# Performance work log

Measured on AMD Instinct MI355X. Metric: run time of the kernel, lower is better.

## Reference

```python
import jax, jax.numpy as jnp
import numpy as np
import math

D, H, DK, F, V, L = 512, 8, 64, 2048, 8192, 2
B, S, T = 16, 128, 128
EPS = 1e-5


def _ln(x, g, b):
    mu = jnp.mean(x, -1, keepdims=True)
    var = jnp.mean((x - mu) ** 2, -1, keepdims=True)
    return g * (x - mu) * jax.lax.rsqrt(var + EPS) + b


def _pe(length):
    pos = jnp.arange(length, dtype=jnp.float32)[:, None]
    div = jnp.exp(jnp.arange(0, D, 2, dtype=jnp.float32) * (-math.log(10000.0) / D))
    ang = pos * div
    pe = jnp.zeros((length, D), jnp.float32)
    return pe.at[:, 0::2].set(jnp.sin(ang)).at[:, 1::2].set(jnp.cos(ang))


def _attn(q, k, v, src, dst, num_dst):
    # per-edge score = exp(clip((k_src . q_dst)/sqrt(d_k), -5, 5))  [E, H]
    score = jnp.einsum('ehd,ehd->eh', k[src], q[dst]) / math.sqrt(DK)
    score = jnp.exp(jnp.clip(score, -5.0, 5.0))
    wv = jax.ops.segment_sum(v[src] * score[..., None], dst, num_segments=num_dst)
    z = jax.ops.segment_sum(score, dst, num_segments=num_dst)
    return (wv / z[..., None]).reshape(num_dst, D)


def _forward(src_tokens, tgt_tokens, ee_src, ee_dst, dd_src, dd_dst, ed_src, ed_dst, P):
    (src_emb, tgt_emb, eW, eB, elg, elb, eW1, eb1, eW2, eb2, eng, enb,
     dsW, dsB, dcW, dcB, dlg, dlb, dW1, db1, dW2, db2, dng, dnb, gW, gb) = P
    pe = _pe(max(S, T))
    Ne, Nd = B * S, B * T
    xe = (src_emb[src_tokens] * math.sqrt(D) + pe[None, :S]).reshape(Ne, D)
    xd = (tgt_emb[tgt_tokens] * math.sqrt(D) + pe[None, :T]).reshape(Nd, D)
    # encoder stack
    for i in range(L):
        nx = _ln(xe, elg[i, 0], elb[i, 0])
        q = (nx @ eW[i, 0] + eB[i, 0]).reshape(Ne, H, DK)
        k = (nx @ eW[i, 1] + eB[i, 1]).reshape(Ne, H, DK)
        v = (nx @ eW[i, 2] + eB[i, 2]).reshape(Ne, H, DK)
        xe = xe + _attn(q, k, v, ee_src, ee_dst, Ne) @ eW[i, 3] + eB[i, 3]
        nx = _ln(xe, elg[i, 1], elb[i, 1])
        xe = xe + jax.nn.relu(nx @ eW1[i] + eb1[i]) @ eW2[i] + eb2[i]
        if i == L - 1:
            xe = _ln(xe, eng, enb)
    # decoder stack
    for i in range(L):
        nx = _ln(xd, dlg[i, 0], dlb[i, 0])
        q = (nx @ dsW[i, 0] + dsB[i, 0]).reshape(Nd, H, DK)
        k = (nx @ dsW[i, 1] + dsB[i, 1]).reshape(Nd, H, DK)
        v = (nx @ dsW[i, 2] + dsB[i, 2]).reshape(Nd, H, DK)
        xd = xd + _attn(q, k, v, dd_src, dd_dst, Nd) @ dsW[i, 3] + dsB[i, 3]
        nq = _ln(xd, dlg[i, 1], dlb[i, 1])
        nkv = _ln(xe, dlg[i, 1], dlb[i, 1])
        q = (nq @ dcW[i, 0] + dcB[i, 0]).reshape(Nd, H, DK)
        k = (nkv @ dcW[i, 1] + dcB[i, 1]).reshape(Ne, H, DK)
        v = (nkv @ dcW[i, 2] + dcB[i, 2]).reshape(Ne, H, DK)
        xd = xd + _attn(q, k, v, ed_src, ed_dst, Nd) @ dcW[i, 3] + dcB[i, 3]
        nx = _ln(xd, dlg[i, 2], dlb[i, 2])
        xd = xd + jax.nn.relu(nx @ dW1[i] + db1[i]) @ dW2[i] + db2[i]
        if i == L - 1:
            xd = _ln(xd, dng, dnb)
    return jax.nn.log_softmax(xd @ gW + gb, axis=-1)  # [Nd, V]


def setup_inputs() -> dict:
    key = jax.random.key(0)
    ks = iter(jax.random.split(key, 40))
    def nrm(shape, scale=0.02):
        return jax.random.normal(next(ks), shape, dtype=jnp.float32) * scale
    src_tokens = jax.random.randint(next(ks), (B, S), 0, V, dtype=jnp.int32)
    tgt_tokens = jax.random.randint(next(ks), (B, T), 0, V, dtype=jnp.int32)
    # graph structure (per-sentence blocks)
    si, di = np.meshgrid(np.arange(S), np.arange(S), indexing='ij')
    si, di = si.ravel(), di.ravel()
    base = (np.arange(B) * S)[:, None]
    ee_src = (base + si[None, :]).ravel().astype(np.int32)
    ee_dst = (base + di[None, :]).ravel().astype(np.int32)
    m = si <= di  # causal: src pos <= dst pos
    dd_src = (base + si[m][None, :]).ravel().astype(np.int32)
    dd_dst = (base + di[m][None, :]).ravel().astype(np.int32)
    ed_src = ee_src.copy()
    ed_dst = ee_dst.copy()
    inp = dict(
        src_tokens=src_tokens, tgt_tokens=tgt_tokens,
        ee_src=jnp.asarray(ee_src), ee_dst=jnp.asarray(ee_dst),
        dd_src=jnp.asarray(dd_src), dd_dst=jnp.asarray(dd_dst),
        ed_src=jnp.asarray(ed_src), ed_dst=jnp.asarray(ed_dst),
        src_emb=nrm((V, D), 1.0 / math.sqrt(D)), tgt_emb=nrm((V, D), 1.0 / math.sqrt(D)),
        enc_attn_W=nrm((L, 4, D, D)), enc_attn_b=jnp.zeros((L, 4, D), jnp.float32),
        enc_ln_g=jnp.ones((L, 2, D), jnp.float32), enc_ln_b=jnp.zeros((L, 2, D), jnp.float32),
        enc_ff_W1=nrm((L, D, F)), enc_ff_b1=jnp.zeros((L, F), jnp.float32),
        enc_ff_W2=nrm((L, F, D)), enc_ff_b2=jnp.zeros((L, D), jnp.float32),
        enc_norm_g=jnp.ones((D,), jnp.float32), enc_norm_b=jnp.zeros((D,), jnp.float32),
        dec_self_W=nrm((L, 4, D, D)), dec_self_b=jnp.zeros((L, 4, D), jnp.float32),
        dec_cross_W=nrm((L, 4, D, D)), dec_cross_b=jnp.zeros((L, 4, D), jnp.float32),
        dec_ln_g=jnp.ones((L, 3, D), jnp.float32), dec_ln_b=jnp.zeros((L, 3, D), jnp.float32),
        dec_ff_W1=nrm((L, D, F)), dec_ff_b1=jnp.zeros((L, F), jnp.float32),
        dec_ff_W2=nrm((L, F, D)), dec_ff_b2=jnp.zeros((L, D), jnp.float32),
        dec_norm_g=jnp.ones((D,), jnp.float32), dec_norm_b=jnp.zeros((D,), jnp.float32),
        gen_W=nrm((D, V)), gen_b=jnp.zeros((V,), jnp.float32),
    )
    return inp


def reference(src_tokens, tgt_tokens, ee_src, ee_dst, dd_src, dd_dst, ed_src, ed_dst,
              src_emb, tgt_emb, enc_attn_W, enc_attn_b, enc_ln_g, enc_ln_b,
              enc_ff_W1, enc_ff_b1, enc_ff_W2, enc_ff_b2, enc_norm_g, enc_norm_b,
              dec_self_W, dec_self_b, dec_cross_W, dec_cross_b, dec_ln_g, dec_ln_b,
              dec_ff_W1, dec_ff_b1, dec_ff_W2, dec_ff_b2, dec_norm_g, dec_norm_b,
              gen_W, gen_b):
    P = (src_emb, tgt_emb, enc_attn_W, enc_attn_b, enc_ln_g, enc_ln_b,
         enc_ff_W1, enc_ff_b1, enc_ff_W2, enc_ff_b2, enc_norm_g, enc_norm_b,
         dec_self_W, dec_self_b, dec_cross_W, dec_cross_b, dec_ln_g, dec_ln_b,
         dec_ff_W1, dec_ff_b1, dec_ff_W2, dec_ff_b2, dec_norm_g, dec_norm_b, gen_W, gen_b)
    return _forward(src_tokens, tgt_tokens, ee_src, ee_dst, dd_src, dd_dst, ed_src, ed_dst, P)
```

## Files before the change

kernel.cpp:

```cpp
#include <hip/hip_runtime.h>

typedef __attribute__((ext_vector_type(8))) short bfx8;
typedef __attribute__((ext_vector_type(4))) float fx4;

static __device__ __forceinline__ unsigned short f2bf(float f) {
    union { float f; unsigned int u; } v; v.f = f;
    unsigned int i = v.u;
    return (unsigned short)((i + 0x7FFFu + ((i >> 16) & 1u)) >> 16);
}
static __device__ __forceinline__ float bf2f(unsigned short u) {
    union { unsigned int ui; float f; } cv;
    cv.ui = ((unsigned int)u) << 16;
    return cv.f;
}

static __device__ __forceinline__ void gl2lds16(const unsigned short* g, unsigned short* l) {
    unsigned long long gu = (unsigned long long)g;
    unsigned int lu = (unsigned int)(unsigned long long)l;
    __builtin_amdgcn_global_load_lds(
        (const __attribute__((address_space(1))) void*)gu,
        (__attribute__((address_space(3))) void*)lu,
        16, 0, 0);
}

struct TrGroup {
    const float* src;
    unsigned short* dst;
    int srcRowStride;
    int dstRowStride;
    long srcSliceOff;
    long dstSliceOff;
};
struct TrTable {
    TrGroup g[18];
    int zStart[19];
};

__global__ __launch_bounds__(256) void trall_kernel(TrTable tt)
{
    __shared__ unsigned short tile[32][33];
    int z = blockIdx.z;
    int gi = 0;
#pragma unroll 1
    while (z >= tt.zStart[gi + 1]) ++gi;
    int zi = z - tt.zStart[gi];
    const float* s = tt.g[gi].src + (size_t)zi * tt.g[gi].srcSliceOff;
    unsigned short* d = tt.g[gi].dst + (size_t)zi * tt.g[gi].dstSliceOff;
    int srs = tt.g[gi].srcRowStride, drs = tt.g[gi].dstRowStride;
    int n0 = blockIdx.x * 32, k0 = blockIdx.y * 32;
    int tx = threadIdx.x & 31, ty = threadIdx.x >> 5;
#pragma unroll
    for (int i = 0; i < 32; i += 8)
        tile[ty + i][tx] = f2bf(s[(size_t)(k0 + ty + i) * srs + (n0 + tx)]);
    __syncthreads();
#pragma unroll
    for (int i = 0; i < 32; i += 8)
        d[(size_t)(n0 + ty + i) * drs + (k0 + tx)] = tile[tx][ty + i];
}

__global__ __launch_bounds__(256) void embed2_kernel(
    const int* __restrict__ tokA, const int* __restrict__ tokB,
    const float* __restrict__ embA, const float* __restrict__ embB,
    float* __restrict__ outA, float* __restrict__ outB)
{
    int idx = blockIdx.x;
    int row = idx & 2047;
    const int* tok = idx < 2048 ? tokA : tokB;
    const float* emb = idx < 2048 ? embA : embB;
    float* out = idx < 2048 ? outA : outB;
    int pos = row & 127;
    int t = tok[row];
    for (int d = threadIdx.x; d < 512; d += 256) {
        float ang = (float)pos * expf((float)(d & ~1) * (-9.210340371976184f / 512.0f));
        float pe = (d & 1) ? cosf(ang) : sinf(ang);
        out[(size_t)row * 512 + d] = emb[(size_t)t * 512 + d] * 22.627416997969522f + pe;
    }
}

static __device__ __forceinline__ void ln_row(
    const float* __restrict__ xrow, const float* __restrict__ g,
    const float* __restrict__ b, int lane, fx4& o0, fx4& o1)
{
    const fx4* xr = (const fx4*)xrow;
    fx4 a = xr[lane * 2], c = xr[lane * 2 + 1];
    float s = a[0] + a[1] + a[2] + a[3] + c[0] + c[1] + c[2] + c[3];
#pragma unroll
    for (int off = 32; off; off >>= 1) s += __shfl_xor(s, off);
    float mu = s * (1.0f / 512.0f);
    float qv = 0.f;
#pragma unroll
    for (int j = 0; j < 4; ++j) {
        float d0 = a[j] - mu; qv += d0 * d0;
        float d1 = c[j] - mu; qv += d1 * d1;
    }
#pragma unroll
    for (int off = 32; off; off >>= 1) qv += __shfl_xor(qv, off);
    float rs = rsqrtf(qv * (1.0f / 512.0f) + 1e-5f);
    const fx4* gr = (const fx4*)g;
    const fx4* br = (const fx4*)b;
    fx4 g0 = gr[lane * 2], g1 = gr[lane * 2 + 1];
    fx4 b0 = br[lane * 2], b1 = br[lane * 2 + 1];
#pragma unroll
    for (int j = 0; j < 4; ++j) {
        o0[j] = g0[j] * (a[j] - mu) * rs + b0[j];
        o1[j] = g1[j] * (c[j] - mu) * rs + b1[j];
    }
}

template<bool OUTBF>
__global__ __launch_bounds__(256) void ln_kernel(
    const float* __restrict__ x, const float* __restrict__ g,
    const float* __restrict__ b, void* __restrict__ out)
{
    int row = blockIdx.x * 4 + (threadIdx.x >> 6);
    int lane = threadIdx.x & 63;
    fx4 o0, o1;
    ln_row(x + (size_t)row * 512, g, b, lane, o0, o1);
    if (OUTBF) {
        unsigned short* orow = (unsigned short*)out + (size_t)row * 512 + lane * 8;
        ushort4 u0 = {f2bf(o0[0]), f2bf(o0[1]), f2bf(o0[2]), f2bf(o0[3])};
        ushort4 u1 = {f2bf(o1[0]), f2bf(o1[1]), f2bf(o1[2]), f2bf(o1[3])};
        *(ushort4*)orow = u0;
        *(ushort4*)(orow + 4) = u1;
    } else {
        fx4* orow = (fx4*)out + (size_t)row * 128;
        orow[lane * 2] = o0;
        orow[lane * 2 + 1] = o1;
    }
}

__global__ __launch_bounds__(256) void ln2_kernel(
    const float* __restrict__ x0, const float* __restrict__ x1,
    const float* __restrict__ g, const float* __restrict__ b,
    unsigned short* __restrict__ o0, unsigned short* __restrict__ o1)
{
    int idx = blockIdx.x * 4 + (threadIdx.x >> 6);
    int lane = threadIdx.x & 63;
    const float* x = idx < 2048 ? x0 : x1;
    unsigned short* o = idx < 2048 ? o0 : o1;
    int row = idx & 2047;
    fx4 v0, v1;
    ln_row(x + (size_t)row * 512, g, b, lane, v0, v1);
    unsigned short* orow = o + (size_t)row * 512 + lane * 8;
    ushort4 u0 = {f2bf(v0[0]), f2bf(v0[1]), f2bf(v0[2]), f2bf(v0[3])};
    ushort4 u1 = {f2bf(v1[0]), f2bf(v1[1]), f2bf(v1[2]), f2bf(v1[3])};
    *(ushort4*)orow = u0;
    *(ushort4*)(orow + 4) = u1;
}

template<bool RELU, bool RESID, bool OUTBF>
__global__ __launch_bounds__(256) void gemm_bk128_kernel(
    const unsigned short* __restrict__ A, const unsigned short* __restrict__ Wt,
    const float* __restrict__ bias, const float* __restrict__ res,
    void* __restrict__ Cv, int K, int ldc, int gx)
{
    __shared__ unsigned short smem[2][2][8192];
    const int tid = threadIdx.x;
    const int nwg = gridDim.x;
    const int cpx = nwg >> 3;
    const int phys = blockIdx.x;
    const int logical = (phys & 7) * cpx + (phys >> 3);
    const int bm = (logical / gx) * 64;
    const int bn = (logical % gx) * 64;
    const int lane = tid & 63;
    const int wv = tid >> 6;
    const int wr = (wv >> 1) * 32;
    const int wc = (wv & 1) * 32;
    const int lr = lane & 15;
    const int lrow4 = lane >> 4;
    const int lchk16 = lane & 15;
    fx4 acc00 = {0.f, 0.f, 0.f, 0.f}, acc01 = {0.f, 0.f, 0.f, 0.f};
    fx4 acc10 = {0.f, 0.f, 0.f, 0.f}, acc11 = {0.f, 0.f, 0.f, 0.f};

    auto stage = [&](int buf, int k0) {
#pragma unroll
        for (int j = 0; j < 4; ++j) {
            int row = wv * 16 + j * 4 + lrow4;
            int sc = (lchk16 ^ (row & 15)) * 8;
            gl2lds16(A + (size_t)(bm + row) * K + k0 + sc,
                     &smem[buf][0][(wv * 16 + j * 4) * 128]);
            gl2lds16(Wt + (size_t)(bn + row) * K + k0 + sc,
                     &smem[buf][1][(wv * 16 + j * 4) * 128]);
        }
    };

    const int nt = K >> 7;
    int cur = 0;
    stage(0, 0);
    for (int t = 0; t < nt; ++t) {
        __syncthreads();
        if (t + 1 < nt) stage(cur ^ 1, (t + 1) << 7);
        const unsigned short* bufA = &smem[cur][0][0];
        const unsigned short* bufB = &smem[cur][1][0];
        const int ra0 = wr + lr, ra1 = wr + 16 + lr;
        const int rb0 = wc + lr, rb1 = wc + 16 + lr;
        __builtin_amdgcn_s_setprio(1);
#pragma unroll
        for (int kk = 0; kk < 4; ++kk) {
            int ca = kk * 4 + (lane >> 4);
            bfx8 a0 = *(const bfx8*)&bufA[ra0 * 128 + ((ca ^ (ra0 & 15)) * 8)];
            bfx8 a1 = *(const bfx8*)&bufA[ra1 * 128 + ((ca ^ (ra1 & 15)) * 8)];
            bfx8 b0 = *(const bfx8*)&bufB[rb0 * 128 + ((ca ^ (rb0 & 15)) * 8)];
            bfx8 b1 = *(const bfx8*)&bufB[rb1 * 128 + ((ca ^ (rb1 & 15)) * 8)];
            acc00 = __builtin_amdgcn_mfma_f32_16x16x32_bf16(a0, b0, acc00, 0, 0, 0);
            acc01 = __builtin_amdgcn_mfma_f32_16x16x32_bf16(a0, b1, acc01, 0, 0, 0);
            acc10 = __builtin_amdgcn_mfma_f32_16x16x32_bf16(a1, b0, acc10, 0, 0, 0);
            acc11 = __builtin_amdgcn_mfma_f32_16x16x32_bf16(a1, b1, acc11, 0, 0, 0);
        }
        __builtin_amdgcn_s_setprio(0);
        cur ^= 1;
    }
    int rbase = bm + wr + ((lane >> 4) * 4);
    int cbase = bn + wc + lr;
#pragma unroll
    for (int m = 0; m < 2; ++m) {
        fx4 am0 = m ? acc10 : acc00;
        fx4 am1 = m ? acc11 : acc01;
#pragma unroll
        for (int r = 0; r < 4; ++r) {
            int row = rbase + m * 16 + r;
#pragma unroll
            for (int half = 0; half < 2; ++half) {
                int col = cbase + half * 16;
                float v = (half ? am1[r] : am0[r]) + bias[col];
                if (RESID) v += res[(size_t)row * ldc + col];
                if (RELU) v = fmaxf(v, 0.f);
                if (OUTBF) ((unsigned short*)Cv)[(size_t)row * ldc + col] = f2bf(v);
                else       ((float*)Cv)[(size_t)row * ldc + col] = v;
            }
        }
    }
}

template<bool RELU>
__global__ __launch_bounds__(256) void gemm128_kernel(
    const unsigned short* __restrict__ A, const unsigned short* __restrict__ Wt,
    const float* __restrict__ bias, unsigned short* __restrict__ C,
    int K, int ldc)
{
    __shared__ unsigned short smem[2][2][8192];
    const int tid = threadIdx.x;
    const int nwg = gridDim.x;
    const int cpx = nwg >> 3;
    const int phys = blockIdx.x;
    const int logical = (phys & 7) * cpx + (phys >> 3);
    const int bm = (logical & 15) * 128;
    const int bn = (logical >> 4) * 128;
    const int lane = tid & 63;
    const int wv = tid >> 6;
    const int wr = (wv >> 1) * 64;
    const int wc = (wv & 1) * 64;
    const int lr = lane & 15;
    const int lrow = lane >> 3;
    const int lchk = lane & 7;
    fx4 acc[4][4];
#pragma unroll
    for (int mi = 0; mi < 4; ++mi)
#pragma unroll
        for (int ni = 0; ni < 4; ++ni) acc[mi][ni] = fx4{0.f, 0.f, 0.f, 0.f};

    auto stage = [&](int buf, int k0) {
#pragma unroll
        for (int j = 0; j < 4; ++j) {
            int row = wv * 32 + j * 8 + lrow;
            int sc = lchk ^ (row & 7);
            gl2lds16(A + (size_t)(bm + row) * K + k0 + sc * 8,
                     &smem[buf][0][(wv * 32 + j * 8) * 64]);
            gl2lds16(Wt + (size_t)(bn + row) * K + k0 + sc * 8,
                     &smem[buf][1][(wv * 32 + j * 8) * 64]);
        }
    };

    const int nt = K >> 6;
    int cur = 0;
    stage(0, 0);
    for (int t = 0; t < nt; ++t) {
        __syncthreads();
        if (t + 1 < nt) stage(cur ^ 1, (t + 1) << 6);
        const unsigned short* bufA = &smem[cur][0][0];
        const unsigned short* bufB = &smem[cur][1][0];
        __builtin_amdgcn_s_setprio(1);
#pragma unroll
        for (int kk = 0; kk < 2; ++kk) {
            int ca = kk * 4 + (lane >> 4);
            bfx8 af[4], bg[4];
#pragma unroll
            for (int i = 0; i < 4; ++i) {
                int ra = wr + i * 16 + lr;
                int rb = wc + i * 16 + lr;
                af[i] = *(const bfx8*)&bufA[ra * 64 + ((ca ^ (ra & 7)) * 8)];
                bg[i] = *(const bfx8*)&bufB[rb * 64 + ((ca ^ (rb & 7)) * 8)];
            }
#pragma unroll
            for (int mi = 0; mi < 4; ++mi)
#pragma unroll
                for (int ni = 0; ni < 4; ++ni)
                    acc[mi][ni] = __builtin_amdgcn_mfma_f32_16x16x32_bf16(af[mi], bg[ni], acc[mi][ni], 0, 0, 0);
        }
        __builtin_amdgcn_s_setprio(0);
        cur ^= 1;
    }
    int rbase = bm + wr + ((lane >> 4) * 4);
    int cbase = bn + wc + lr;
#pragma unroll
    for (int mi = 0; mi < 4; ++mi)
#pragma unroll
        for (int ni = 0; ni < 4; ++ni) {
            int col = cbase + ni * 16;
            float bv = bias[col];
#pragma unroll
            for (int r = 0; r < 4; ++r) {
                int row = rbase + mi * 16 + r;
                float v = acc[mi][ni][r] + bv;
                if (RELU) v = fmaxf(v, 0.f);
                C[(size_t)row * ldc + col] = f2bf(v);
            }
        }
}

template<bool CAUSAL, bool SELF>
__global__ __launch_bounds__(512) void fattn_kernel(
    const unsigned short* __restrict__ xq, const unsigned short* __restrict__ xkv,
    const unsigned short* __restrict__ Wt, const float* __restrict__ bias,
    unsigned short* __restrict__ out)
{
    constexpr int XROWS = SELF ? 128 : 192;
    constexpr int BUFB  = (XROWS + 192) * 64 * 2;
    __shared__ __align__(16) unsigned char lds[2 * BUFB + 9216 + 18432 + 17408 + 512];
    const int blk = blockIdx.x;
    const int half = blk & 1;
    const int h = (blk >> 1) & 7;
    const int b = blk >> 4;
    const int q0 = half * 64;
    const int tid = threadIdx.x;
    const int lane = tid & 63;
    const int wv = tid >> 6;
    const int lr = lane & 15;
    const int hg8 = (lane >> 4) * 8;
    const int rloc = (lane >> 4) * 4;
    const int lrow = lane >> 3;
    const int lchk = lane & 7;

    const unsigned short* gxq = xq + (size_t)(b * 128 + q0) * 512;
    const unsigned short* gkv = xkv + (size_t)(b * 128) * 512;
    const unsigned short* gw  = Wt + (size_t)(h * 64) * 512;

    auto stage = [&](int buf, int k0) {
        unsigned short* dst = (unsigned short*)(lds + buf * BUFB);
        if constexpr (SELF) {
#pragma unroll
            for (int j = 0; j < 5; ++j) {
                int start = wv * 40 + j * 8;
                int row = start + lrow;
                int sc = (lchk ^ (row & 7)) * 8;
                const unsigned short* src;
                if (start < 128) {
                    src = gkv + (size_t)row * 512 + k0 + sc;
                } else {
                    int wr_ = row - 128;
                    src = gw + ((size_t)(wr_ & 63) + (size_t)(wr_ >> 6) * 512) * 512 + k0 + sc;
                }
                gl2lds16(src, dst + start * 64);
            }
        } else {
            unsigned short* dstW = dst + XROWS * 64;
#pragma unroll
            for (int j = 0; j < 3; ++j) {
                int row = wv * 24 + j * 8 + lrow;
                int sc = (lchk ^ (row & 7)) * 8;
                const unsigned short* xs = (row < 64)
                    ? gxq + (size_t)row * 512
                    : gkv + (size_t)(row - 64) * 512;
                gl2lds16(xs + k0 + sc, dst + (wv * 24 + j * 8) * 64);
                const unsigned short* ws = gw + ((size_t)(row & 63) + (size_t)(row >> 6) * 512) * 512;
                gl2lds16(ws + k0 + sc, dstW + (wv * 24 + j * 8) * 64);
            }
        }
    };

    fx4 accQ[4], accK[4], accV[4];
#pragma unroll
    for (int c = 0; c < 4; ++c) {
        accQ[c] = fx4{0.f, 0.f, 0.f, 0.f};
        accK[c] = fx4{0.f, 0.f, 0.f, 0.f};
        accV[c] = fx4{0.f, 0.f, 0.f, 0.f};
    }
    stage(0, 0);
#pragma unroll 1
    for (int t = 0; t < 8; ++t) {
        __syncthreads();
        if (t < 7) stage((t + 1) & 1, (t + 1) * 64);
        const unsigned short* stX = (const unsigned short*)(lds + (t & 1) * BUFB);
        const unsigned short* stW = stX + XROWS * 64;
#pragma unroll
        for (int kk = 0; kk < 2; ++kk) {
            const int ca = kk * 4 + (lane >> 4);
            auto rd = [&](const unsigned short* base, int row) -> bfx8 {
                return *(const bfx8*)(base + row * 64 + ((ca ^ (row & 7)) * 8));
            };
            const int kvbase = SELF ? 0 : 64;
            bfx8 aKV = rd(stX, kvbase + wv * 16 + lr);
            bfx8 aQ = aKV;
            if (wv >= 4) aQ = rd(stX, (SELF ? q0 : 0) + (wv - 4) * 16 + lr);
            __builtin_amdgcn_s_setprio(1);
#pragma unroll
            for (int c = 0; c < 4; ++c) {
                bfx8 bk = rd(stW, 64 + c * 16 + lr);
                accK[c] = __builtin_amdgcn_mfma_f32_16x16x32_bf16(aKV, bk, accK[c], 0, 0, 0);
                bfx8 bv = rd(stW, 128 + c * 16 + lr);
                accV[c] = __builtin_amdgcn_mfma_f32_16x16x32_bf16(aKV, bv, accV[c], 0, 0, 0);
                if (wv >= 4) {
                    bfx8 bq = rd(stW, c * 16 + lr);
                    accQ[c] = __builtin_amdgcn_mfma_f32_16x16x32_bf16(aQ, bq, accQ[c], 0, 0, 0);
                }
            }
            __builtin_amdgcn_s_setprio(0);
        }
    }
    unsigned short* sQ  = (unsigned short*)(lds + 2 * BUFB);
    unsigned short* sK  = (unsigned short*)(lds + 2 * BUFB + 9216);
    unsigned short* sVt = (unsigned short*)(lds + 2 * BUFB + 9216 + 18432);
    float* zp = (float*)(lds + 2 * BUFB + 9216 + 18432 + 17408);
    unsigned short* sP  = (unsigned short*)lds;
#pragma unroll
    for (int c = 0; c < 4; ++c) {
        int col = c * 16 + lr;
        float bk_ = bias[512 + h * 64 + col];
        float bv_ = bias[1024 + h * 64 + col];
#pragma unroll
        for (int r = 0; r < 4; ++r) {
            sK[(wv * 16 + rloc + r) * 72 + col] = f2bf(accK[c][r] + bk_);
            sVt[col * 136 + (wv * 16 + rloc + r)] = f2bf(accV[c][r] + bv_);
        }
        if (wv >= 4) {
            float bq_ = bias[h * 64 + col];
#pragma unroll
            for (int r = 0; r < 4; ++r)
                sQ[((wv - 4) * 16 + rloc + r) * 72 + col] = f2bf(accQ[c][r] + bq_);
        }
    }
    __syncthreads();
    const int qb = wv >> 1;
    const int kh = wv & 1;
    fx4 acc[4];
#pragma unroll
    for (int n = 0; n < 4; ++n) acc[n] = fx4{0.f, 0.f, 0.f, 0.f};
#pragma unroll
    for (int kk = 0; kk < 2; ++kk) {
        bfx8 a = *(const bfx8*)(sQ + (qb * 16 + lr) * 72 + kk * 32 + hg8);
#pragma unroll
        for (int n = 0; n < 4; ++n) {
            bfx8 bb = *(const bfx8*)(sK + ((kh * 4 + n) * 16 + lr) * 72 + kk * 32 + hg8);
            acc[n] = __builtin_amdgcn_mfma_f32_16x16x32_bf16(a, bb, acc[n], 0, 0, 0);
        }
    }
    const int qg = q0 + qb * 16 + rloc;
#pragma unroll
    for (int r = 0; r < 4; ++r) {
        float zs = 0.f;
#pragma unroll
        for (int n = 0; n < 4; ++n) {
            float s = acc[n][r] * 0.125f;
            s = __expf(fminf(fmaxf(s, -5.f), 5.f));
            if (CAUSAL && (kh * 64 + n * 16 + lr) > (qg + r)) s = 0.f;
            zs += s;
            sP[(qb * 16 + rloc + r) * 136 + kh * 64 + n * 16 + lr] = f2bf(s);
        }
#pragma unroll
        for (int off = 8; off; off >>= 1) zs += __shfl_xor(zs, off);
        if (lr == 0) zp[(qb * 2 + kh) * 16 + rloc + r] = zs;
    }
    __syncthreads();
    float zinv[4];
#pragma unroll
    for (int r = 0; r < 4; ++r)
        zinv[r] = 1.f / (zp[(qb * 2 + 0) * 16 + rloc + r] + zp[(qb * 2 + 1) * 16 + rloc + r]);
    const int dh = wv & 1;
    fx4 acc2[2];
    acc2[0] = fx4{0.f, 0.f, 0.f, 0.f};
    acc2[1] = fx4{0.f, 0.f, 0.f, 0.f};
#pragma unroll
    for (int kk = 0; kk < 4; ++kk) {
        bfx8 a = *(const bfx8*)(sP + (qb * 16 + lr) * 136 + kk * 32 + hg8);
#pragma unroll
        for (int dn = 0; dn < 2; ++dn) {
            bfx8 bb = *(const bfx8*)(sVt + (dh * 32 + dn * 16 + lr) * 136 + kk * 32 + hg8);
            acc2[dn] = __builtin_amdgcn_mfma_f32_16x16x32_bf16(a, bb, acc2[dn], 0, 0, 0);
        }
    }
#pragma unroll
    for (int dn = 0; dn < 2; ++dn)
#pragma unroll
        for (int r = 0; r < 4; ++r) {
            size_t row = (size_t)(b * 128 + qg + r);
            out[row * 512 + h * 64 + dh * 32 + dn * 16 + lr] = f2bf(acc2[dn][r] * zinv[r]);
        }
}

__global__ __launch_bounds__(256) void logsoftmax_bf16_kernel(
    const unsigned short* __restrict__ logits, float* __restrict__ out)
{
    __shared__ float red[4];
    int tid = threadIdx.x;
    const bfx8* lrow = (const bfx8*)(logits + (size_t)blockIdx.x * 8192);
    float* orow = out + (size_t)blockIdx.x * 8192;
    float vals[32];
    float mx = -1e30f;
#pragma unroll
    for (int i = 0; i < 4; ++i) {
        bfx8 u = lrow[i * 256 + tid];
#pragma unroll
        for (int j = 0; j < 8; ++j) {
            float f = bf2f((unsigned short)u[j]);
            vals[i * 8 + j] = f;
            mx = fmaxf(mx, f);
        }
    }
#pragma unroll
    for (int off = 32; off; off >>= 1) mx = fmaxf(mx, __shfl_xor(mx, off));
    int wid = tid >> 6;
    if ((tid & 63) == 0) red[wid] = mx;
    __syncthreads();
    mx = fmaxf(fmaxf(red[0], red[1]), fmaxf(red[2], red[3]));
    __syncthreads();
    float sum = 0.f;
#pragma unroll
    for (int i = 0; i < 32; ++i) sum += __expf(vals[i] - mx);
#pragma unroll
    for (int off = 32; off; off >>= 1) sum += __shfl_xor(sum, off);
    if ((tid & 63) == 0) red[wid] = sum;
    __syncthreads();
    sum = red[0] + red[1] + red[2] + red[3];
    float lsub = mx + logf(sum);
#pragma unroll
    for (int i = 0; i < 4; ++i) {
        fx4 o0, o1;
#pragma unroll
        for (int j = 0; j < 4; ++j) {
            o0[j] = vals[i * 8 + j] - lsub;
            o1[j] = vals[i * 8 + 4 + j] - lsub;
        }
        ((fx4*)orow)[(i * 256 + tid) * 2] = o0;
        ((fx4*)orow)[(i * 256 + tid) * 2 + 1] = o1;
    }
}

extern "C" void kernel_launch(void* const* d_in, const int* in_sizes, int n_in,
                              void* d_out, int out_size, void* d_ws, size_t ws_size,
                              hipStream_t stream) {
    (void)in_sizes; (void)n_in; (void)out_size; (void)ws_size;
    const int* src_tokens = (const int*)d_in[0];
    const int* tgt_tokens = (const int*)d_in[1];
    const float* src_emb    = (const float*)d_in[8];
    const float* tgt_emb    = (const float*)d_in[9];
    const float* enc_attn_W = (const float*)d_in[10];
    const float* enc_attn_b = (const float*)d_in[11];
    const float* enc_ln_g   = (const float*)d_in[12];
    const float* enc_ln_b   = (const float*)d_in[13];
    const float* enc_ff_W1  = (const float*)d_in[14];
    const float* enc_ff_b1  = (const float*)d_in[15];
    const float* enc_ff_W2  = (const float*)d_in[16];
    const float* enc_ff_b2  = (const float*)d_in[17];
    const float* enc_norm_g = (const float*)d_in[18];
    const float* enc_norm_b = (const float*)d_in[19];
    const float* dec_self_W = (const float*)d_in[20];
    const float* dec_self_b = (const float*)d_in[21];
    const float* dec_cross_W= (const float*)d_in[22];
    const float* dec_cross_b= (const float*)d_in[23];
    const float* dec_ln_g   = (const float*)d_in[24];
    const float* dec_ln_b   = (const float*)d_in[25];
    const float* dec_ff_W1  = (const float*)d_in[26];
    const float* dec_ff_b1  = (const float*)d_in[27];
    const float* dec_ff_W2  = (const float*)d_in[28];
    const float* dec_ff_b2  = (const float*)d_in[29];
    const float* dec_norm_g = (const float*)d_in[30];
    const float* dec_norm_b = (const float*)d_in[31];
    const float* gen_W      = (const float*)d_in[32];
    const float* gen_b      = (const float*)d_in[33];
    float* dout = (float*)d_out;

    unsigned short* wt = (unsigned short*)d_ws;
    const size_t OFF_ENCQKV = 0;
    const size_t OFF_ENCO   = 1572864;
    const size_t OFF_ENCW1  = 2097152;
    const size_t OFF_ENCW2  = 4194304;
    const size_t OFF_DECSQKV= 6291456;
    const size_t OFF_DECSO  = 7864320;
    const size_t OFF_DECCQKV= 8388608;
    const size_t OFF_DECCO  = 9961472;
    const size_t OFF_DECW1  = 10485760;
    const size_t OFF_DECW2  = 12582912;
    const size_t OFF_GENW   = 14680064;
    const size_t WT_ELEMS   = 18874368;
    float* fb  = (float*)(wt + WT_ELEMS);
    float* xe  = fb;
    float* xd  = fb + 1048576;
    unsigned short* nxb  = (unsigned short*)(fb + 2097152);
    unsigned short* nkvb = (unsigned short*)(fb + 3145728);
    unsigned short* ffb  = (unsigned short*)(fb + 4194304);
    unsigned short* attb = (unsigned short*)(fb + 7340032);
    unsigned short* genin   = (unsigned short*)fb;
    unsigned short* logitsb = (unsigned short*)(fb + 1048576);

    TrTable tt;
    {
        int z = 0, gi = 0;
        auto addg = [&](const float* s, unsigned short* d, int srs, int drs,
                        long so, long dof, int zc) {
            tt.zStart[gi] = z;
            tt.g[gi].src = s; tt.g[gi].dst = d;
            tt.g[gi].srcRowStride = srs; tt.g[gi].dstRowStride = drs;
            tt.g[gi].srcSliceOff = so; tt.g[gi].dstSliceOff = dof;
            ++gi; z += zc;
        };
        addg(enc_attn_W,              wt + OFF_ENCQKV,               512,  512,  262144,    262144, 3);
        addg(enc_attn_W + 4L*262144,  wt + OFF_ENCQKV + 3L*262144,   512,  512,  262144,    262144, 3);
        addg(enc_attn_W + 3L*262144,  wt + OFF_ENCO,                 512,  512,  4L*262144, 262144, 2);
        addg(enc_ff_W1,               wt + OFF_ENCW1,                2048, 512,  512,       262144, 4);
        addg(enc_ff_W1 + 1048576,     wt + OFF_ENCW1 + 1048576,      2048, 512,  512,       262144, 4);
        addg(enc_ff_W2,               wt + OFF_ENCW2,                512,  2048, 262144,    512,    4);
        addg(enc_ff_W2 + 1048576,     wt + OFF_ENCW2 + 1048576,      512,  2048, 262144,    512,    4);
        addg(dec_self_W,              wt + OFF_DECSQKV,              512,  512,  262144,    262144, 3);
        addg(dec_self_W + 4L*262144,  wt + OFF_DECSQKV + 3L*262144,  512,  512,  262144,    262144, 3);
        addg(dec_self_W + 3L*262144,  wt + OFF_DECSO,                512,  512,  4L*262144, 262144, 2);
        addg(dec_cross_W,             wt + OFF_DECCQKV,              512,  512,  262144,    262144, 3);
        addg(dec_cross_W + 4L*262144, wt + OFF_DECCQKV + 3L*262144,  512,  512,  262144,    262144, 3);
        addg(dec_cross_W + 3L*262144, wt + OFF_DECCO,                512,  512,  4L*262144, 262144, 2);
        addg(dec_ff_W1,               wt + OFF_DECW1,                2048, 512,  512,       262144, 4);
        addg(dec_ff_W1 + 1048576,     wt + OFF_DECW1 + 1048576,      2048, 512,  512,       262144, 4);
        addg(dec_ff_W2,               wt + OFF_DECW2,                512,  2048, 262144,    512,    4);
        addg(dec_ff_W2 + 1048576,     wt + OFF_DECW2 + 1048576,      512,  2048, 262144,    512,    4);
        addg(gen_W,                   wt + OFF_GENW,                 8192, 512,  512,       262144, 16);
        tt.zStart[18] = z;
    }
    trall_kernel<<<dim3(16, 16, 72), 256, 0, stream>>>(tt);

    embed2_kernel<<<4096, 256, 0, stream>>>(src_tokens, tgt_tokens, src_emb, tgt_emb, xe, xd);

    auto gemmK = [&](const unsigned short* A, const unsigned short* W, const float* bias,
                     const float* res, void* C, int N, int K, int ldc, bool relu, bool outbf) {
        int gx = N / 64;
        dim3 g(gx * 32);
        if (res)        gemm_bk128_kernel<false, true,  false><<<g, 256, 0, stream>>>(A, W, bias, res, C, K, ldc, gx);
        else if (relu)  gemm_bk128_kernel<true,  false, true ><<<g, 256, 0, stream>>>(A, W, bias, res, C, K, ldc, gx);
        else if (outbf) gemm_bk128_kernel<false, false, true ><<<g, 256, 0, stream>>>(A, W, bias, res, C, K, ldc, gx);
        else            gemm_bk128_kernel<false, false, false><<<g, 256, 0, stream>>>(A, W, bias, res, C, K, ldc, gx);
    };
    auto gemm128 = [&](const unsigned short* A, const unsigned short* W, const float* bias,
                       unsigned short* C, int N, int K, int ldc, bool relu) {
        dim3 g((N / 128) * 16);
        if (relu) gemm128_kernel<true ><<<g, 256, 0, stream>>>(A, W, bias, C, K, ldc);
        else      gemm128_kernel<false><<<g, 256, 0, stream>>>(A, W, bias, C, K, ldc);
    };
    auto lnb = [&](const float* x, const float* g, const float* b, unsigned short* o) {
        ln_kernel<true><<<512, 256, 0, stream>>>(x, g, b, o);
    };
    auto lnf = [&](const float* x, const float* g, const float* b, float* o) {
        ln_kernel<false><<<512, 256, 0, stream>>>(x, g, b, o);
    };

    for (int i = 0; i < 2; ++i) {
        lnb(xe, enc_ln_g + (size_t)(i * 2 + 0) * 512, enc_ln_b + (size_t)(i * 2 + 0) * 512, nxb);
        fattn_kernel<false, true><<<256, 512, 0, stream>>>(
            nxb, nxb, wt + OFF_ENCQKV + (size_t)i * 3 * 262144,
            enc_attn_b + (size_t)i * 4 * 512, attb);
        gemmK(attb, wt + OFF_ENCO + (size_t)i * 262144, enc_attn_b + (size_t)i * 4 * 512 + 1536,
              xe, xe, 512, 512, 512, false, false);
        lnb(xe, enc_ln_g + (size_t)(i * 2 + 1) * 512, enc_ln_b + (size_t)(i * 2 + 1) * 512, nxb);
        gemm128(nxb, wt + OFF_ENCW1 + (size_t)i * 1048576, enc_ff_b1 + (size_t)i * 2048,
                ffb, 2048, 512, 2048, true);
        gemmK(ffb, wt + OFF_ENCW2 + (size_t)i * 1048576, enc_ff_b2 + (size_t)i * 512,
              xe, xe, 512, 2048, 512, false, false);
    }
    lnf(xe, enc_norm_g, enc_norm_b, xe);

    for (int i = 0; i < 2; ++i) {
        lnb(xd, dec_ln_g + (size_t)(i * 3 + 0) * 512, dec_ln_b + (size_t)(i * 3 + 0) * 512, nxb);
        fattn_kernel<true, true><<<256, 512, 0, stream>>>(
            nxb, nxb, wt + OFF_DECSQKV + (size_t)i * 3 * 262144,
            dec_self_b + (size_t)i * 4 * 512, attb);
        gemmK(attb, wt + OFF_DECSO + (size_t)i * 262144, dec_self_b + (size_t)i * 4 * 512 + 1536,
              xd, xd, 512, 512, 512, false, false);
        ln2_kernel<<<1024, 256, 0, stream>>>(
            xd, xe, dec_ln_g + (size_t)(i * 3 + 1) * 512, dec_ln_b + (size_t)(i * 3 + 1) * 512,
            nxb, nkvb);
        fattn_kernel<false, false><<<256, 512, 0, stream>>>(
            nxb, nkvb, wt + OFF_DECCQKV + (size_t)i * 3 * 262144,
            dec_cross_b + (size_t)i * 4 * 512, attb);
        gemmK(attb, wt + OFF_DECCO + (size_t)i * 262144, dec_cross_b + (size_t)i * 4 * 512 + 1536,
              xd, xd, 512, 512, 512, false, false);
        lnb(xd, dec_ln_g + (size_t)(i * 3 + 2) * 512, dec_ln_b + (size_t)(i * 3 + 2) * 512, nxb);
        gemm128(nxb, wt + OFF_DECW1 + (size_t)i * 1048576, dec_ff_b1 + (size_t)i * 2048,
                ffb, 2048, 512, 2048, true);
        gemmK(ffb, wt + OFF_DECW2 + (size_t)i * 1048576, dec_ff_b2 + (size_t)i * 512,
              xd, xd, 512, 2048, 512, false, false);
    }
    lnb(xd, dec_norm_g, dec_norm_b, genin);

    gemm128(genin, wt + OFF_GENW, gen_b, logitsb, 8192, 512, 8192, false);
    logsoftmax_bf16_kernel<<<2048, 256, 0, stream>>>(logitsb, dout);
}
```

Measured before the change: 336.7 us.

## Fuse LayerNorm into embedding, output-projection GEMMs, and encoder final norm

Embedding now also computes the first encoder and decoder LayerNorms. A new full-row GEMM kernel (64x512 tile) fuses bias, residual and the following LayerNorm for the attention output projections. The encoder final norm also produces both decoder cross-attention K/V LayerNorm outputs up front. This removes several separate LN launches and the re-read of the residual stream. In exchange, the fused GEMM launches only 32 workgroups, which may underuse the GPU, and it computes variance as E[x²]−mu² in single-pass form.

```diff
diff --git a/kernel.cpp b/kernel.cpp
--- a/kernel.cpp
+++ b/kernel.cpp
@@ -58,23 +58,51 @@
         d[(size_t)(n0 + ty + i) * drs + (k0 + tx)] = tile[tx][ty + i];
 }
 
-__global__ __launch_bounds__(256) void embed2_kernel(
+__global__ __launch_bounds__(256) void embedln_kernel(
     const int* __restrict__ tokA, const int* __restrict__ tokB,
     const float* __restrict__ embA, const float* __restrict__ embB,
-    float* __restrict__ outA, float* __restrict__ outB)
+    float* __restrict__ outA, float* __restrict__ outB,
+    const float* __restrict__ gA, const float* __restrict__ bA,
+    const float* __restrict__ gB, const float* __restrict__ bB,
+    unsigned short* __restrict__ nxA, unsigned short* __restrict__ nxB)
 {
+    __shared__ float red[4];
     int idx = blockIdx.x;
     int row = idx & 2047;
-    const int* tok = idx < 2048 ? tokA : tokB;
-    const float* emb = idx < 2048 ? embA : embB;
-    float* out = idx < 2048 ? outA : outB;
+    bool e = idx < 2048;
+    const int* tok = e ? tokA : tokB;
+    const float* emb = e ? embA : embB;
+    float* out = e ? outA : outB;
+    const float* g = e ? gA : gB;
+    const float* bb = e ? bA : bB;
+    unsigned short* nx = e ? nxA : nxB;
     int pos = row & 127;
     int t = tok[row];
-    for (int d = threadIdx.x; d < 512; d += 256) {
+    int d0 = threadIdx.x, d1 = threadIdx.x + 256;
+    auto pe = [&](int d) {
         float ang = (float)pos * expf((float)(d & ~1) * (-9.210340371976184f / 512.0f));
-        float pe = (d & 1) ? cosf(ang) : sinf(ang);
-        out[(size_t)row * 512 + d] = emb[(size_t)t * 512 + d] * 22.627416997969522f + pe;
-    }
+        return (d & 1) ? cosf(ang) : sinf(ang);
+    };
+    float v0 = emb[(size_t)t * 512 + d0] * 22.627416997969522f + pe(d0);
+    float v1 = emb[(size_t)t * 512 + d1] * 22.627416997969522f + pe(d1);
+    out[(size_t)row * 512 + d0] = v0;
+    out[(size_t)row * 512 + d1] = v1;
+    int lane = threadIdx.x & 63, wv = threadIdx.x >> 6;
+    float s = v0 + v1;
+#pragma unroll
+    for (int off = 32; off; off >>= 1) s += __shfl_xor(s, off);
+    if (lane == 0) red[wv] = s;
+    __syncthreads();
+    float mu = (red[0] + red[1] + red[2] + red[3]) * (1.0f / 512.0f);
+    __syncthreads();
+    float q = (v0 - mu) * (v0 - mu) + (v1 - mu) * (v1 - mu);
+#pragma unroll
+    for (int off = 32; off; off >>= 1) q += __shfl_xor(q, off);
+    if (lane == 0) red[wv] = q;
+    __syncthreads();
+    float rs = rsqrtf((red[0] + red[1] + red[2] + red[3]) * (1.0f / 512.0f) + 1e-5f);
+    nx[(size_t)row * 512 + d0] = f2bf(g[d0] * (v0 - mu) * rs + bb[d0]);
+    nx[(size_t)row * 512 + d1] = f2bf(g[d1] * (v1 - mu) * rs + bb[d1]);
 }
 
 static __device__ __forceinline__ void ln_row(
@@ -129,23 +157,51 @@
     }
 }
 
-__global__ __launch_bounds__(256) void ln2_kernel(
-    const float* __restrict__ x0, const float* __restrict__ x1,
-    const float* __restrict__ g, const float* __restrict__ b,
-    unsigned short* __restrict__ o0, unsigned short* __restrict__ o1)
+__global__ __launch_bounds__(256) void ln3_kernel(
+    float* __restrict__ xe, const float* __restrict__ eg, const float* __restrict__ eb,
+    const float* __restrict__ g0, const float* __restrict__ b0,
+    const float* __restrict__ g1, const float* __restrict__ b1,
+    unsigned short* __restrict__ nk0, unsigned short* __restrict__ nk1)
 {
-    int idx = blockIdx.x * 4 + (threadIdx.x >> 6);
+    int row = blockIdx.x * 4 + (threadIdx.x >> 6);
     int lane = threadIdx.x & 63;
-    const float* x = idx < 2048 ? x0 : x1;
-    unsigned short* o = idx < 2048 ? o0 : o1;
-    int row = idx & 2047;
-    fx4 v0, v1;
-    ln_row(x + (size_t)row * 512, g, b, lane, v0, v1);
-    unsigned short* orow = o + (size_t)row * 512 + lane * 8;
-    ushort4 u0 = {f2bf(v0[0]), f2bf(v0[1]), f2bf(v0[2]), f2bf(v0[3])};
-    ushort4 u1 = {f2bf(v1[0]), f2bf(v1[1]), f2bf(v1[2]), f2bf(v1[3])};
-    *(ushort4*)orow = u0;
-    *(ushort4*)(orow + 4) = u1;
+    fx4 t0, t1;
+    ln_row(xe + (size_t)row * 512, eg, eb, lane, t0, t1);
+    fx4* orow = (fx4*)(xe + (size_t)row * 512);
+    orow[lane * 2] = t0;
+    orow[lane * 2 + 1] = t1;
+    float s = t0[0] + t0[1] + t0[2] + t0[3] + t1[0] + t1[1] + t1[2] + t1[3];
+#pragma unroll
+    for (int off = 32; off; off >>= 1) s += __shfl_xor(s, off);
+    float mu = s * (1.0f / 512.0f);
+    float q = 0.f;
+#pragma unroll
+    for (int j = 0; j < 4; ++j) {
+        float a = t0[j] - mu; q += a * a;
+        float c = t1[j] - mu; q += c * c;
+    }
+#pragma unroll
+    for (int off = 32; off; off >>= 1) q += __shfl_xor(q, off);
+    float rs = rsqrtf(q * (1.0f / 512.0f) + 1e-5f);
+    const fx4* g0r = (const fx4*)g0; const fx4* b0r = (const fx4*)b0;
+    const fx4* g1r = (const fx4*)g1; const fx4* b1r = (const fx4*)b1;
+    fx4 ga0 = g0r[lane * 2], ga1 = g0r[lane * 2 + 1];
+    fx4 bb0 = b0r[lane * 2], bb1 = b0r[lane * 2 + 1];
+    fx4 gc0 = g1r[lane * 2], gc1 = g1r[lane * 2 + 1];
+    fx4 bc0 = b1r[lane * 2], bc1 = b1r[lane * 2 + 1];
+    unsigned short* o0 = nk0 + (size_t)row * 512 + lane * 8;
+    unsigned short* o1 = nk1 + (size_t)row * 512 + lane * 8;
+    ushort4 ua0, ua1, uc0, uc1;
+#pragma unroll
+    for (int j = 0; j < 4; ++j) {
+        float n0 = (t0[j] - mu) * rs, n1 = (t1[j] - mu) * rs;
+        ((unsigned short*)&ua0)[j] = f2bf(ga0[j] * n0 + bb0[j]);
+        ((unsigned short*)&ua1)[j] = f2bf(ga1[j] * n1 + bb1[j]);
+        ((unsigned short*)&uc0)[j] = f2bf(gc0[j] * n0 + bc0[j]);
+        ((unsigned short*)&uc1)[j] = f2bf(gc1[j] * n1 + bc1[j]);
+    }
+    *(ushort4*)o0 = ua0; *(ushort4*)(o0 + 4) = ua1;
+    *(ushort4*)o1 = uc0; *(ushort4*)(o1 + 4) = uc1;
 }
 
 template<bool RELU, bool RESID, bool OUTBF>
@@ -230,6 +286,146 @@
             }
         }
     }
+}
+
+__global__ __launch_bounds__(256) void gemm_ln_kernel(
+    const unsigned short* __restrict__ A, const unsigned short* __restrict__ Wt,
+    const float* __restrict__ bias, float* __restrict__ res,
+    const float* __restrict__ lgam, const float* __restrict__ lbet,
+    unsigned short* __restrict__ lnout)
+{
+    __shared__ unsigned short sA[2][4096];
+    __shared__ unsigned short sB[2][32768];
+    __shared__ float redS[64][4];
+    __shared__ float redQ[64][4];
+    __shared__ float murs[64][2];
+    const int tid = threadIdx.x;
+    const int bm = blockIdx.x * 64;
+    const int lane = tid & 63;
+    const int wv = tid >> 6;
+    const int lr = lane & 15;
+    const int g4 = (lane >> 4) * 4;
+    const int lrow = lane >> 3;
+    const int lchk = lane & 7;
+
+    fx4 acc[4][8];
+#pragma unroll
+    for (int m = 0; m < 4; ++m)
+#pragma unroll
+        for (int n = 0; n < 8; ++n) acc[m][n] = fx4{0.f, 0.f, 0.f, 0.f};
+
+    float bias_c[8], gam_c[8], bet_c[8];
+#pragma unroll
+    for (int n = 0; n < 8; ++n) {
+        int col = wv * 128 + n * 16 + lr;
+        bias_c[n] = bias[col];
+        gam_c[n] = lgam[col];
+        bet_c[n] = lbet[col];
+    }
+
+    auto stage = [&](int buf, int k0) {
+#pragma unroll
+        for (int j = 0; j < 2; ++j) {
+            int row = wv * 16 + j * 8 + lrow;
+            int sc = lchk ^ (row & 7);
+            gl2lds16(A + (size_t)(bm + row) * 512 + k0 + sc * 8,
+                     &sA[buf][(wv * 16 + j * 8) * 64]);
+        }
+#pragma unroll
+        for (int j = 0; j < 16; ++j) {
+            int row = wv * 128 + j * 8 + lrow;
+            int sc = lchk ^ (row & 7);
+            gl2lds16(Wt + (size_t)row * 512 + k0 + sc * 8,
+                     &sB[buf][(wv * 128 + j * 8) * 64]);
+        }
+    };
+
+    stage(0, 0);
+#pragma unroll 1
+    for (int t = 0; t < 8; ++t) {
+        __syncthreads();
+        if (t < 7) stage((t + 1) & 1, (t + 1) * 64);
+        const unsigned short* bA = sA[t & 1];
+        const unsigned short* bB = sB[t & 1];
+        __builtin_amdgcn_s_setprio(1);
+#pragma unroll
+        for (int kk = 0; kk < 2; ++kk) {
+            int ca = kk * 4 + (lane >> 4);
+            bfx8 af[4], bf_[8];
+#pragma unroll
+            for (int m = 0; m < 4; ++m) {
+                int r = m * 16 + lr;
+                af[m] = *(const bfx8*)&bA[r * 64 + ((ca ^ (r & 7)) * 8)];
+            }
+#pragma unroll
+            for (int n = 0; n < 8; ++n) {
+                int r = wv * 128 + n * 16 + lr;
+                bf_[n] = *(const bfx8*)&bB[r * 64 + ((ca ^ (r & 7)) * 8)];
+            }
+#pragma unroll
+            for (int m = 0; m < 4; ++m)
+#pragma unroll
+                for (int n = 0; n < 8; ++n)
+                    acc[m][n] = __builtin_amdgcn_mfma_f32_16x16x32_bf16(af[m], bf_[n], acc[m][n], 0, 0, 0);
+        }
+        __builtin_amdgcn_s_setprio(0);
+    }
+#pragma unroll
+    for (int m = 0; m < 4; ++m)
+#pragma unroll
+        for (int n = 0; n < 8; ++n) {
+            int col = wv * 128 + n * 16 + lr;
+#pragma unroll
+            for (int r = 0; r < 4; ++r) {
+                size_t grow = bm + m * 16 + g4 + r;
+                acc[m][n][r] += bias_c[n] + res[grow * 512 + col];
+            }
+        }
+#pragma unroll
+    for (int m = 0; m < 4; ++m)
+#pragma unroll
+        for (int r = 0; r < 4; ++r) {
+            float s1 = 0.f, s2 = 0.f;
+#pragma unroll
+            for (int n = 0; n < 8; ++n) {
+                float x = acc[m][n][r];
+                s1 += x; s2 += x * x;
+            }
+#pragma unroll
+            for (int off = 8; off; off >>= 1) {
+                s1 += __shfl_xor(s1, off);
+                s2 += __shfl_xor(s2, off);
+            }
+            if (lr == 0) {
+                redS[m * 16 + g4 + r][wv] = s1;
+                redQ[m * 16 + g4 + r][wv] = s2;
+            }
+        }
+    __syncthreads();
+    if (tid < 64) {
+        float s1 = redS[tid][0] + redS[tid][1] + redS[tid][2] + redS[tid][3];
+        float s2 = redQ[tid][0] + redQ[tid][1] + redQ[tid][2] + redQ[tid][3];
+        float mu = s1 * (1.0f / 512.0f);
+        float var = s2 * (1.0f / 512.0f) - mu * mu;
+        murs[tid][0] = mu;
+        murs[tid][1] = rsqrtf(var + 1e-5f);
+    }
+    __syncthreads();
+#pragma unroll
+    for (int m = 0; m < 4; ++m)
+#pragma unroll
+        for (int r = 0; r < 4; ++r) {
+            int rl = m * 16 + g4 + r;
+            float mu = murs[rl][0], rs = murs[rl][1];
+            size_t grow = bm + rl;
+#pragma unroll
+            for (int n = 0; n < 8; ++n) {
+                int col = wv * 128 + n * 16 + lr;
+                float x = acc[m][n][r];
+                res[grow * 512 + col] = x;
+                lnout[grow * 512 + col] = f2bf(gam_c[n] * (x - mu) * rs + bet_c[n]);
+            }
+        }
 }
 
 template<bool RELU>
@@ -595,10 +791,12 @@
     float* fb  = (float*)(wt + WT_ELEMS);
     float* xe  = fb;
     float* xd  = fb + 1048576;
-    unsigned short* nxb  = (unsigned short*)(fb + 2097152);
-    unsigned short* nkvb = (unsigned short*)(fb + 3145728);
-    unsigned short* ffb  = (unsigned short*)(fb + 4194304);
-    unsigned short* attb = (unsigned short*)(fb + 7340032);
+    unsigned short* nxb   = (unsigned short*)(fb + 2097152);
+    unsigned short* nxd0  = (unsigned short*)(fb + 3145728);
+    unsigned short* ffb   = (unsigned short*)(fb + 4194304);
+    unsigned short* nkvb0 = (unsigned short*)(fb + 6291456);
+    unsigned short* nkvb1 = (unsigned short*)(fb + 6815744);
+    unsigned short* attb  = (unsigned short*)(fb + 7340032);
     unsigned short* genin   = (unsigned short*)fb;
     unsigned short* logitsb = (unsigned short*)(fb + 1048576);
 
@@ -635,7 +833,9 @@
     }
     trall_kernel<<<dim3(16, 16, 72), 256, 0, stream>>>(tt);
 
-    embed2_kernel<<<4096, 256, 0, stream>>>(src_tokens, tgt_tokens, src_emb, tgt_emb, xe, xd);
+    embedln_kernel<<<4096, 256, 0, stream>>>(
+        src_tokens, tgt_tokens, src_emb, tgt_emb, xe, xd,
+        enc_ln_g, enc_ln_b, dec_ln_g, dec_ln_b, nxb, nxd0);
 
     auto gemmK = [&](const unsigned short* A, const unsigned short* W, const float* bias,
                      const float* res, void* C, int N, int K, int ldc, bool relu, bool outbf) {
@@ -645,6 +845,10 @@
         else if (relu)  gemm_bk128_kernel<true,  false, true ><<<g, 256, 0, stream>>>(A, W, bias, res, C, K, ldc, gx);
         else if (outbf) gemm_bk128_kernel<false, false, true ><<<g, 256, 0, stream>>>(A, W, bias, res, C, K, ldc, gx);
         else            gemm_bk128_kernel<false, false, false><<<g, 256, 0, stream>>>(A, W, bias, res, C, K, ldc, gx);
+    };
+    auto gemmLN = [&](const unsigned short* A, const unsigned short* W, const float* bias,
+                      float* res, const float* lg, const float* lb, unsigned short* lnout) {
+        gemm_ln_kernel<<<32, 256, 0, stream>>>(A, W, bias, res, lg, lb, lnout);
     };
     auto gemm128 = [&](const unsigned short* A, const unsigned short* W, const float* bias,
                        unsigned short* C, int N, int K, int ldc, bool relu) {
@@ -655,41 +859,38 @@
     auto lnb = [&](const float* x, const float* g, const float* b, unsigned short* o) {
         ln_kernel<true><<<512, 256, 0, stream>>>(x, g, b, o);
     };
-    auto lnf = [&](const float* x, const float* g, const float* b, float* o) {
-        ln_kernel<false><<<512, 256, 0, stream>>>(x, g, b, o);
-    };
 
     for (int i = 0; i < 2; ++i) {
-        lnb(xe, enc_ln_g + (size_t)(i * 2 + 0) * 512, enc_ln_b + (size_t)(i * 2 + 0) * 512, nxb);
+        if (i) lnb(xe, enc_ln_g + (size_t)(i * 2) * 512, enc_ln_b + (size_t)(i * 2) * 512, nxb);
         fattn_kernel<false, true><<<256, 512, 0, stream>>>(
             nxb, nxb, wt + OFF_ENCQKV + (size_t)i * 3 * 262144,
             enc_attn_b + (size_t)i * 4 * 512, attb);
-        gemmK(attb, wt + OFF_ENCO + (size_t)i * 262144, enc_attn_b + (size_t)i * 4 * 512 + 1536,
-              xe, xe, 512, 512, 512, false, false);
-        lnb(xe, enc_ln_g + (size_t)(i * 2 + 1) * 512, enc_ln_b + (size_t)(i * 2 + 1) * 512, nxb);
+        gemmLN(attb, wt + OFF_ENCO + (size_t)i * 262144, enc_attn_b + (size_t)i * 4 * 512 + 1536,
+               xe, enc_ln_g + (size_t)(i * 2 + 1) * 512, enc_ln_b + (size_t)(i * 2 + 1) * 512, nxb);
         gemm128(nxb, wt + OFF_ENCW1 + (size_t)i * 1048576, enc_ff_b1 + (size_t)i * 2048,
                 ffb, 2048, 512, 2048, true);
         gemmK(ffb, wt + OFF_ENCW2 + (size_t)i * 1048576, enc_ff_b2 + (size_t)i * 512,
               xe, xe, 512, 2048, 512, false, false);
     }
-    lnf(xe, enc_norm_g, enc_norm_b, xe);
+    ln3_kernel<<<512, 256, 0, stream>>>(
+        xe, enc_norm_g, enc_norm_b,
+        dec_ln_g + 512, dec_ln_b + 512,
+        dec_ln_g + 4 * 512, dec_ln_b + 4 * 512,
+        nkvb0, nkvb1);
 
     for (int i = 0; i < 2; ++i) {
-        lnb(xd, dec_ln_g + (size_t)(i * 3 + 0) * 512, dec_ln_b + (size_t)(i * 3 + 0) * 512, nxb);
+        const unsigned short* qsrc = (i == 0) ? nxd0 : nxb;
+        if (i) lnb(xd, dec_ln_g + (size_t)(i * 3) * 512, dec_ln_b + (size_t)(i * 3) * 512, nxb);
         fattn_kernel<true, true><<<256, 512, 0, stream>>>(
-            nxb, nxb, wt + OFF_DECSQKV + (size_t)i * 3 * 262144,
+            qsrc, qsrc, wt + OFF_DECSQKV + (size_t)i * 3 * 262144,
             dec_self_b + (size_t)i * 4 * 512, attb);
-        gemmK(attb, wt + OFF_DECSO + (size_t)i * 262144, dec_self_b + (size_t)i * 4 * 512 + 1536,
-              xd, xd, 512, 512, 512, false, false);
-        ln2_kernel<<<1024, 256, 0, stream>>>(
-            xd, xe, dec_ln_g + (size_t)(i * 3 + 1) * 512, dec_ln_b + (size_t)(i * 3 + 1) * 512,
-            nxb, nkvb);
+        gemmLN(attb, wt + OFF_DECSO + (size_t)i * 262144, dec_self_b + (size_t)i * 4 * 512 + 1536,
+               xd, dec_ln_g + (size_t)(i * 3 + 1) * 512, dec_ln_b + (size_t)(i * 3 + 1) * 512, nxb);
         fattn_kernel<false, false><<<256, 512, 0, stream>>>(
-            nxb, nkvb, wt + OFF_DECCQKV + (size_t)i * 3 * 262144,
+            nxb, i ? nkvb1 : nkvb0, wt + OFF_DECCQKV + (size_t)i * 3 * 262144,
             dec_cross_b + (size_t)i * 4 * 512, attb);
-        gemmK(attb, wt + OFF_DECCO + (size_t)i * 262144, dec_cross_b + (size_t)i * 4 * 512 + 1536,
-              xd, xd, 512, 512, 512, false, false);
-        lnb(xd, dec_ln_g + (size_t)(i * 3 + 2) * 512, dec_ln_b + (size_t)(i * 3 + 2) * 512, nxb);
+        gemmLN(attb, wt + OFF_DECCO + (size_t)i * 262144, dec_cross_b + (size_t)i * 4 * 512 + 1536,
+               xd, dec_ln_g + (size_t)(i * 3 + 2) * 512, dec_ln_b + (size_t)(i * 3 + 2) * 512, nxb);
         gemm128(nxb, wt + OFF_DECW1 + (size_t)i * 1048576, dec_ff_b1 + (size_t)i * 2048,
                 ffb, 2048, 512, 2048, true);
         gemmK(ffb, wt + OFF_DECW2 + (size_t)i * 1048576, dec_ff_b2 + (size_t)i * 512,
```

After: 408.1 us. 21.2% more time.
